# Kernel tuning notes

Measured on AMD Instinct MI355X. Metric: run time of the kernel, lower is better.

Reference implementation:

```python
import jax, jax.numpy as jnp
import numpy as np

H_HEADS = 8  # num_heads

def _layernorm(x, w, b, eps=1e-5):
    mu = x.mean(-1, keepdims=True)
    var = ((x - mu) ** 2).mean(-1, keepdims=True)
    return (x - mu) / jnp.sqrt(var + eps) * w + b

def _encoder(h, qkv_w, qkv_b, out_w, out_b, ln1_w, ln1_b, ln2_w, ln2_b, ff1_w, ff1_b, ff2_w, ff2_b):
    # h: [G, n, E]; post-norm TransformerEncoderLayer (PyTorch default, eval mode)
    G, n, E = h.shape
    hd = E // H_HEADS
    for l in range(qkv_w.shape[0]):
        qkv = h @ qkv_w[l].T + qkv_b[l]                       # [G, n, 3E]
        q, k, v = jnp.split(qkv, 3, axis=-1)
        q = q.reshape(G, n, H_HEADS, hd).transpose(0, 2, 1, 3)
        k = k.reshape(G, n, H_HEADS, hd).transpose(0, 2, 1, 3)
        v = v.reshape(G, n, H_HEADS, hd).transpose(0, 2, 1, 3)
        att = jax.nn.softmax(jnp.einsum('ghqd,ghkd->ghqk', q, k) / jnp.sqrt(jnp.float32(hd)), axis=-1)
        o = jnp.einsum('ghqk,ghkd->ghqd', att, v).transpose(0, 2, 1, 3).reshape(G, n, E)
        o = o @ out_w[l].T + out_b[l]
        h = _layernorm(h + o, ln1_w[l], ln1_b[l])
        ff = jax.nn.relu(h @ ff1_w[l].T + ff1_b[l]) @ ff2_w[l].T + ff2_b[l]
        h = _layernorm(h + ff, ln2_w[l], ln2_b[l])
    return h

def setup_inputs():
    G, N, D_IN, E, L, DFF, NE, K = 64, 512, 128, 256, 4, 2048, 524288, 128
    key = jax.random.key(0)
    ks = jax.random.split(key, 12)
    s = 0.02
    return {
        'x': jax.random.normal(ks[0], (G * N, D_IN), jnp.float32),
        'edge_index': jax.random.randint(ks[1], (2, NE), 0, G * N, dtype=jnp.int32),
        'edge_weights': jax.random.uniform(ks[2], (NE,), jnp.float32),
        'emb_w': jax.random.normal(ks[3], (E, D_IN), jnp.float32) * s,
        'emb_b': jnp.zeros((E,), jnp.float32),
        'qkv_w': jax.random.normal(ks[4], (L, 3 * E, E), jnp.float32) * s,
        'qkv_b': jnp.zeros((L, 3 * E), jnp.float32),
        'out_w': jax.random.normal(ks[5], (L, E, E), jnp.float32) * s,
        'out_b': jnp.zeros((L, E), jnp.float32),
        'ln1_w': jnp.ones((L, E), jnp.float32),
        'ln1_b': jnp.zeros((L, E), jnp.float32),
        'ln2_w': jnp.ones((L, E), jnp.float32),
        'ln2_b': jnp.zeros((L, E), jnp.float32),
        'ff1_w': jax.random.normal(ks[6], (L, DFF, E), jnp.float32) * s,
        'ff1_b': jnp.zeros((L, DFF), jnp.float32),
        'ff2_w': jax.random.normal(ks[7], (L, E, DFF), jnp.float32) * s,
        'ff2_b': jnp.zeros((L, E), jnp.float32),
        'score_w': jax.random.normal(ks[8], (1, E), jnp.float32) * s,
        'score_b': jnp.zeros((1,), jnp.float32),
        'num_graphs': 64,
        'k': 128,
    }

def reference(x, edge_index, edge_weights, emb_w, emb_b, qkv_w, qkv_b, out_w, out_b,
              ln1_w, ln1_b, ln2_w, ln2_b, ff1_w, ff1_b, ff2_w, ff2_b, score_w, score_b,
              num_graphs, k):
    GN = x.shape[0]
    n = GN // num_graphs           # uniform graph size -> node_mask == arange(G).repeat(n)
    E = emb_w.shape[0]
    h = (x @ emb_w.T + emb_b).reshape(num_graphs, n, E)
    h = _encoder(h, qkv_w, qkv_b, out_w, out_b, ln1_w, ln1_b, ln2_w, ln2_b,
                 ff1_w, ff1_b, ff2_w, ff2_b)
    scores = (h.reshape(GN, E) @ score_w.T + score_b)[:, 0]      # [GN]
    probs = jax.nn.sigmoid(scores)
    # per-graph top-k (topk_fix: k = min(sample_abs, n))
    vals, idx = jax.lax.top_k(probs.reshape(num_graphs, n), k)   # [G, k]
    full_idx = (idx + jnp.arange(num_graphs)[:, None] * n).reshape(-1)
    probs_new = jnp.zeros_like(probs).at[full_idx].set(vals.reshape(-1))
    mask = (probs_new != 0).astype(probs.dtype)
    # straight-through: indexes = detach(mask - probs) + probs; probs = probs * indexes
    indexes = jax.lax.stop_gradient(mask - probs) + probs
    probs_f = probs * indexes
    ew = edge_weights * probs_f[edge_index[0]] * probs_f[edge_index[1]]
    sampled_nodes = jnp.sort(full_idx)
    return ew, sampled_nodes, probs_f
```

## Files before the change

### kernel.cpp

```cpp
#include <hip/hip_runtime.h>
#include <cstdint>
#include <cstddef>

#define GN    32768
#define GG    64
#define NNODE 512
#define EE    256
#define LL    4
#define DFFN  2048
#define NHH   8
#define HD    32
#define NEDGE 524288
#define KSEL  128
#define DIN   128

typedef __attribute__((ext_vector_type(8))) short short8;
typedef __attribute__((ext_vector_type(4))) float floatx4;

__device__ __forceinline__ unsigned short f2bf(float x) {
  unsigned u = __float_as_uint(x);
  u = (u + 0x7FFFu + ((u >> 16) & 1u)) >> 16;
  return (unsigned short)u;
}
__device__ __forceinline__ float bf2f(unsigned short u) {
  return __uint_as_float((unsigned)u << 16);
}
__device__ __forceinline__ unsigned tpack(float v) {
  unsigned hib = __float_as_uint(v) & 0xFFFF0000u;
  float hif = __uint_as_float(hib);
  unsigned pk;
  asm("v_cvt_pk_bf16_f32 %0, %1, %2" : "=v"(pk) : "v"(hif), "v"(v - hif));
  return pk;
}
__device__ __forceinline__ unsigned short bf1(float v) {
  unsigned pk;
  asm("v_cvt_pk_bf16_f32 %0, %1, %2" : "=v"(pk) : "v"(v), "v"(0.0f));
  return (unsigned short)pk;
}
__device__ __forceinline__ void unpk(uint4 a0, uint4 a1, short8& hi, short8& lo) {
  union { short8 s; unsigned u[4]; } H, L;
  H.u[0] = __builtin_amdgcn_perm(a0.y, a0.x, 0x05040100u);
  H.u[1] = __builtin_amdgcn_perm(a0.w, a0.z, 0x05040100u);
  H.u[2] = __builtin_amdgcn_perm(a1.y, a1.x, 0x05040100u);
  H.u[3] = __builtin_amdgcn_perm(a1.w, a1.z, 0x05040100u);
  L.u[0] = __builtin_amdgcn_perm(a0.y, a0.x, 0x07060302u);
  L.u[1] = __builtin_amdgcn_perm(a0.w, a0.z, 0x07060302u);
  L.u[2] = __builtin_amdgcn_perm(a1.y, a1.x, 0x07060302u);
  L.u[3] = __builtin_amdgcn_perm(a1.w, a1.z, 0x07060302u);
  hi = H.s; lo = L.s;
}

__device__ __forceinline__ void ld_lds16(const ushort* g, ushort* l) {
  __builtin_amdgcn_global_load_lds(
      (const __attribute__((address_space(1))) unsigned int*)g,
      (__attribute__((address_space(3))) unsigned int*)l, 16, 0, 0);
}

__global__ __launch_bounds__(256) void split_kernel(const float* __restrict__ in,
                                                    ushort* __restrict__ hi,
                                                    ushort* __restrict__ lo, int n4) {
  int i = blockIdx.x * 256 + threadIdx.x;
  if (i >= n4) return;
  float4 v = ((const float4*)in)[i];
  ushort4 hv, lv;
  float t[4] = {v.x, v.y, v.z, v.w};
  unsigned short hb;
  hb = f2bf(t[0]); hv.x = hb; lv.x = f2bf(t[0] - bf2f(hb));
  hb = f2bf(t[1]); hv.y = hb; lv.y = f2bf(t[1] - bf2f(hb));
  hb = f2bf(t[2]); hv.z = hb; lv.z = f2bf(t[2] - bf2f(hb));
  hb = f2bf(t[3]); hv.w = hb; lv.w = f2bf(t[3] - bf2f(hb));
  ((ushort4*)hi)[i] = hv;
  ((ushort4*)lo)[i] = lv;
}

__global__ __launch_bounds__(256) void split_qkvw(const float* __restrict__ in,
                                                  ushort* __restrict__ hi,
                                                  ushort* __restrict__ lo, int n4) {
  int i = blockIdx.x * 256 + threadIdx.x;
  if (i >= n4) return;
  float4 v = ((const float4*)in)[i];
  int row = (i >> 6) % 768;
  float sc = (row < 256) ? (0.17677669529663687f * 1.44269504088896340f) : 1.0f;
  float t[4] = {v.x * sc, v.y * sc, v.z * sc, v.w * sc};
  ushort4 hv, lv;
  unsigned short hb;
  hb = f2bf(t[0]); hv.x = hb; lv.x = f2bf(t[0] - bf2f(hb));
  hb = f2bf(t[1]); hv.y = hb; lv.y = f2bf(t[1] - bf2f(hb));
  hb = f2bf(t[2]); hv.z = hb; lv.z = f2bf(t[2] - bf2f(hb));
  hb = f2bf(t[3]); hv.w = hb; lv.w = f2bf(t[3] - bf2f(hb));
  ((ushort4*)hi)[i] = hv;
  ((ushort4*)lo)[i] = lv;
}

__global__ __launch_bounds__(256) void scale_qb(const float* __restrict__ qb,
                                                float* __restrict__ outb) {
  int i = blockIdx.x * 256 + threadIdx.x;
  if (i >= LL * 768) return;
  float sc = ((i % 768) < 256) ? (0.17677669529663687f * 1.44269504088896340f) : 1.0f;
  outb[i] = qb[i] * sc;
}

template <int BM, int BN, int MODE, bool RELU, bool VT, bool ACC,
          bool PACKA = false, bool PACKC = false, bool SINGA = false,
          bool SINGC = false>
__global__ __launch_bounds__(256) void mm_split(
    const ushort* __restrict__ a_hi, const ushort* __restrict__ a_lo,
    const ushort* __restrict__ b_hi, const ushort* __restrict__ b_lo,
    const float* __restrict__ bias,
    float* __restrict__ Cf, ushort* __restrict__ c_hi, ushort* __restrict__ c_lo,
    ushort* __restrict__ vth, ushort* __restrict__ vtl,
    int M, int N, int K, int lda, int ldb) {
  constexpr int MI = BM / 32;
  constexpr int NJ = BN / 32;
  constexpr int APL = SINGA ? 1 : 2;
  __shared__ ushort As[2][APL][BM * 32];
  __shared__ ushort Bs[2][2][BN * 32];
  const int tid = threadIdx.x;
  const int w = tid >> 6, lane = tid & 63;
  const int wm = (w >> 1) * (BM / 2), wn = (w & 1) * (BN / 2);

  const int nwg = gridDim.x * gridDim.y;
  int flat = blockIdx.x + gridDim.x * blockIdx.y;
  int bnb, bmb;
  if ((nwg & 7) == 0) {
    int v = (flat & 7) * (nwg >> 3) + (flat >> 3);
    bnb = v % gridDim.x;
    bmb = v / gridDim.x;
  } else {
    bnb = blockIdx.x;
    bmb = blockIdx.y;
  }
  const int bm = bmb * BM, bn = bnb * BN;
  const int lrow = lane & 15, lquad = lane >> 4;

  floatx4 acc[MI][NJ];
  floatx4 zz = {0.f, 0.f, 0.f, 0.f};
#pragma unroll
  for (int i = 0; i < MI; ++i)
#pragma unroll
    for (int j = 0; j < NJ; ++j) acc[i][j] = zz;

  const uint* aP = (const uint*)a_hi;
  const int arow = tid >> 2;
  const int acol = (((tid & 3) ^ ((arow >> 1) & 3)) << 3);
  const ushort* pah = a_hi + (size_t)(bm + arow) * lda + acol;
  const ushort* pal = a_lo + (size_t)(bm + arow) * lda + acol;
  const ushort* pbh = b_hi + (size_t)(bn + arow) * ldb + acol;
  const ushort* pbl = b_lo + (size_t)(bn + arow) * ldb + acol;

  auto stage = [&](int p, int k0) {
    if constexpr (PACKA) {
#pragma unroll
      for (int s = 0; s < BM / 32; ++s) {
        int row = s * 32 + (tid >> 3);
        int gp = tid & 7;
        const uint* src = aP + (size_t)(bm + row) * lda + k0 + ((gp ^ (row & 7)) << 2);
        ld_lds16((const ushort*)src,
                 (ushort*)((char*)&As[p][0][0] + s * 4096 + tid * 16));
      }
    } else {
#pragma unroll
      for (int s = 0; s < BM / 64; ++s) {
        ld_lds16(pah + (size_t)s * 64 * lda + k0, &As[p][0][s * 2048 + tid * 8]);
        if constexpr (!SINGA)
          ld_lds16(pal + (size_t)s * 64 * lda + k0, &As[p][1][s * 2048 + tid * 8]);
      }
    }
#pragma unroll
    for (int s = 0; s < BN / 64; ++s) {
      ld_lds16(pbh + (size_t)s * 64 * ldb + k0, &Bs[p][0][s * 2048 + tid * 8]);
      ld_lds16(pbl + (size_t)s * 64 * ldb + k0, &Bs[p][1][s * 2048 + tid * 8]);
    }
  };

  stage(0, 0);
  const int nk = K >> 5;
  for (int t = 0; t < nk; ++t) {
    const int p = t & 1;
    __syncthreads();
    if (t + 1 < nk) stage(p ^ 1, (t + 1) << 5);
    short8 ah[MI], al[MI], bh[NJ], bl[NJ];
    if constexpr (PACKA) {
      const uint* Ap = (const uint*)&As[p][0][0];
#pragma unroll
      for (int i = 0; i < MI; ++i) {
        int rr = wm + i * 16 + lrow;
        const uint* rb = Ap + rr * 32;
        uint4 a0 = *(const uint4*)(rb + (((lquad * 2) ^ (rr & 7)) << 2));
        uint4 a1 = *(const uint4*)(rb + (((lquad * 2 + 1) ^ (rr & 7)) << 2));
        unpk(a0, a1, ah[i], al[i]);
      }
    } else {
#pragma unroll
      for (int i = 0; i < MI; ++i) {
        int rr = wm + i * 16 + lrow;
        int r = rr * 32 + ((lquad ^ ((rr >> 1) & 3)) << 3);
        ah[i] = *(const short8*)&As[p][0][r];
        if constexpr (!SINGA) al[i] = *(const short8*)&As[p][1][r];
      }
    }
#pragma unroll
    for (int j = 0; j < NJ; ++j) {
      int rr = wn + j * 16 + lrow;
      int r = rr * 32 + ((lquad ^ ((rr >> 1) & 3)) << 3);
      bh[j] = *(const short8*)&Bs[p][0][r];
      bl[j] = *(const short8*)&Bs[p][1][r];
    }
#pragma unroll
    for (int i = 0; i < MI; ++i)
#pragma unroll
      for (int j = 0; j < NJ; ++j) {
        if constexpr (SINGA) {
          acc[i][j] = __builtin_amdgcn_mfma_f32_16x16x32_bf16(ah[i], bl[j], acc[i][j], 0, 0, 0);
          acc[i][j] = __builtin_amdgcn_mfma_f32_16x16x32_bf16(ah[i], bh[j], acc[i][j], 0, 0, 0);
        } else {
          acc[i][j] = __builtin_amdgcn_mfma_f32_16x16x32_bf16(al[i], bh[j], acc[i][j], 0, 0, 0);
          acc[i][j] = __builtin_amdgcn_mfma_f32_16x16x32_bf16(ah[i], bl[j], acc[i][j], 0, 0, 0);
          acc[i][j] = __builtin_amdgcn_mfma_f32_16x16x32_bf16(ah[i], bh[j], acc[i][j], 0, 0, 0);
        }
      }
  }

#pragma unroll
  for (int j = 0; j < NJ; ++j) {
    int col = bn + wn + j * 16 + lrow;
    float bj = ACC ? 0.0f : bias[col];
#pragma unroll
    for (int i = 0; i < MI; ++i) {
      int row0 = bm + wm + i * 16 + lquad * 4;
#pragma unroll
      for (int r = 0; r < 4; ++r) {
        size_t off = (size_t)(row0 + r) * N + col;
        float v = acc[i][j][r] + bj;
        if constexpr (ACC) v += Cf[off];
        if (RELU) v = fmaxf(v, 0.0f);
        if constexpr (MODE & 1) Cf[off] = v;
        if constexpr (SINGC) {
          c_hi[off] = bf1(v);
        } else if constexpr (PACKC) {
          if constexpr (VT) {
            if (col < 512) {
              ((uint*)c_hi)[off] = tpack(v);
            } else {
              int hd = col - 512;
              int row = row0 + r;
              size_t vo = ((size_t)((row >> 9) * 8 + (hd >> 5)) * 32 + (hd & 31)) * 512 + (row & 511);
              vth[vo] = bf1(v);
            }
          } else {
            ((uint*)c_hi)[off] = tpack(v);
          }
        } else if constexpr (MODE & 2) {
          unsigned short hb = f2bf(v);
          unsigned short lb = f2bf(v - bf2f(hb));
          c_hi[off] = hb;
          c_lo[off] = lb;
        }
      }
    }
  }
}

__global__ __launch_bounds__(256) void mm_ln(
    const uint* __restrict__ oP,
    const ushort* __restrict__ b_hi, const ushort* __restrict__ b_lo,
    const float* __restrict__ bias, const float* __restrict__ lnw,
    const float* __restrict__ lnb, float* __restrict__ hbuf,
    uint* __restrict__ hP, int K) {
  __shared__ uint AsP[32 * 32];
  __shared__ ushort Bs[2][256 * 32];
  __shared__ float rsum[32], rsq[32], muA[32], rsA[32];
  const int tid = threadIdx.x;
  const int w = tid >> 6, lane = tid & 63;
  const int wn = w * 64;
  const int bm = blockIdx.x * 32;
  const int lr = lane & 15, quad = lane >> 4;

  floatx4 acc[2][4];
  floatx4 zz = {0.f, 0.f, 0.f, 0.f};
#pragma unroll
  for (int i = 0; i < 2; ++i)
#pragma unroll
    for (int j = 0; j < 4; ++j) acc[i][j] = zz;

  if (tid < 32) { rsum[tid] = 0.f; rsq[tid] = 0.f; }

  const int brow = tid >> 2;
  const int bcol = (((tid & 3) ^ ((brow >> 1) & 3)) << 3);

  for (int k0 = 0; k0 < K; k0 += 32) {
    __syncthreads();
    {
      int row = tid >> 3, gp = tid & 7;
      const uint* src = oP + (size_t)(bm + row) * 256 + k0 + ((gp ^ (row & 7)) << 2);
      ld_lds16((const ushort*)src, (ushort*)((char*)AsP + tid * 16));
    }
#pragma unroll
    for (int s = 0; s < 4; ++s) {
      ld_lds16(b_hi + (size_t)(s * 64 + brow) * K + bcol + k0, &Bs[0][s * 2048 + tid * 8]);
      ld_lds16(b_lo + (size_t)(s * 64 + brow) * K + bcol + k0, &Bs[1][s * 2048 + tid * 8]);
    }
    __syncthreads();
    short8 ah[2], al[2], bh[4], bl[4];
#pragma unroll
    for (int i = 0; i < 2; ++i) {
      int rr = i * 16 + lr;
      const uint* rb = AsP + rr * 32;
      uint4 a0 = *(const uint4*)(rb + (((quad * 2) ^ (rr & 7)) << 2));
      uint4 a1 = *(const uint4*)(rb + (((quad * 2 + 1) ^ (rr & 7)) << 2));
      unpk(a0, a1, ah[i], al[i]);
    }
#pragma unroll
    for (int j = 0; j < 4; ++j) {
      int rr = wn + j * 16 + lr;
      int r = rr * 32 + ((quad ^ ((rr >> 1) & 3)) << 3);
      bh[j] = *(const short8*)&Bs[0][r];
      bl[j] = *(const short8*)&Bs[1][r];
    }
#pragma unroll
    for (int i = 0; i < 2; ++i)
#pragma unroll
      for (int j = 0; j < 4; ++j) {
        acc[i][j] = __builtin_amdgcn_mfma_f32_16x16x32_bf16(al[i], bh[j], acc[i][j], 0, 0, 0);
        acc[i][j] = __builtin_amdgcn_mfma_f32_16x16x32_bf16(ah[i], bl[j], acc[i][j], 0, 0, 0);
        acc[i][j] = __builtin_amdgcn_mfma_f32_16x16x32_bf16(ah[i], bh[j], acc[i][j], 0, 0, 0);
      }
  }

#pragma unroll
  for (int i = 0; i < 2; ++i) {
#pragma unroll
    for (int r = 0; r < 4; ++r) {
      int ridx = i * 16 + quad * 4 + r;
      float sp = 0.f, qp = 0.f;
#pragma unroll
      for (int j = 0; j < 4; ++j) {
        int col = wn + j * 16 + lr;
        float v = acc[i][j][r] + bias[col] + hbuf[(size_t)(bm + ridx) * EE + col];
        acc[i][j][r] = v;
        sp += v;
        qp += v * v;
      }
#pragma unroll
      for (int m = 1; m < 16; m <<= 1) { sp += __shfl_xor(sp, m); qp += __shfl_xor(qp, m); }
      if (lr == 0) { atomicAdd(&rsum[ridx], sp); atomicAdd(&rsq[ridx], qp); }
    }
  }
  __syncthreads();
  if (tid < 32) {
    float mu = rsum[tid] * (1.0f / 256.0f);
    float var = rsq[tid] * (1.0f / 256.0f) - mu * mu;
    muA[tid] = mu;
    rsA[tid] = 1.0f / sqrtf(var + 1e-5f);
  }
  __syncthreads();
#pragma unroll
  for (int i = 0; i < 2; ++i) {
#pragma unroll
    for (int r = 0; r < 4; ++r) {
      int ridx = i * 16 + quad * 4 + r;
      float mu = muA[ridx], rsv = rsA[ridx];
#pragma unroll
      for (int j = 0; j < 4; ++j) {
        int col = wn + j * 16 + lr;
        float o = (acc[i][j][r] - mu) * rsv * lnw[col] + lnb[col];
        size_t off = (size_t)(bm + ridx) * EE + col;
        hbuf[off] = o;
        hP[off] = tpack(o);
      }
    }
  }
}

__global__ __launch_bounds__(256) void ln_res_kernel(float* __restrict__ h,
                                                     const float* __restrict__ t,
                                                     const float* __restrict__ w,
                                                     const float* __restrict__ b,
                                                     uint* __restrict__ hP) {
  int row = blockIdx.x * 4 + (threadIdx.x >> 6);
  int lane = threadIdx.x & 63;
  size_t off = (size_t)row * EE + (lane << 2);
  float4 hv = *(const float4*)&h[off];
  float4 tv = *(const float4*)&t[off];
  float v0 = hv.x + tv.x, v1 = hv.y + tv.y, v2 = hv.z + tv.z, v3 = hv.w + tv.w;
  float s = (v0 + v1) + (v2 + v3);
#pragma unroll
  for (int m = 32; m > 0; m >>= 1) s += __shfl_xor(s, m);
  float mu = s * (1.0f / 256.0f);
  float d0 = v0 - mu, d1 = v1 - mu, d2 = v2 - mu, d3 = v3 - mu;
  float s2 = (d0 * d0 + d1 * d1) + (d2 * d2 + d3 * d3);
#pragma unroll
  for (int m = 32; m > 0; m >>= 1) s2 += __shfl_xor(s2, m);
  float rs = 1.0f / sqrtf(s2 * (1.0f / 256.0f) + 1e-5f);
  float4 wv = *(const float4*)&w[lane << 2];
  float4 bv = *(const float4*)&b[lane << 2];
  float4 o;
  o.x = d0 * rs * wv.x + bv.x;
  o.y = d1 * rs * wv.y + bv.y;
  o.z = d2 * rs * wv.z + bv.z;
  o.w = d3 * rs * wv.w + bv.w;
  *(float4*)&h[off] = o;
  uint4 pk;
  pk.x = tpack(o.x);
  pk.y = tpack(o.y);
  pk.z = tpack(o.z);
  pk.w = tpack(o.w);
  *(uint4*)&hP[off] = pk;
}

__global__ __launch_bounds__(256) void attn_mfma(const uint* __restrict__ qP,
                                                 const ushort* __restrict__ vtS,
                                                 uint* __restrict__ oP) {
  __shared__ ushort Ks[2][64 * 40];
  __shared__ ushort Vt[32 * 72];
  __shared__ ushort Ps[4][16 * 72];
  const int tid = threadIdx.x;
  const int w = tid >> 6, lane = tid & 63, c = lane & 15, quad = lane >> 4;
  int flat = blockIdx.x + 8 * (blockIdx.y + 8 * blockIdx.z);
  int v = (flat & 7) * ((GG * 64) >> 3) + (flat >> 3);
  const int qt = v & 7, hh = (v >> 3) & 7, g = v >> 6;
  const size_t g512 = (size_t)g * 512;
  const size_t vtbase = (size_t)(g * 8 + hh) * 32 * 512;

  const size_t qnode = g512 + qt * 64 + w * 16 + c;
  const uint* qp0 = qP + qnode * 768 + hh * 32 + quad * 8;
  uint4 q0 = *(const uint4*)qp0, q1 = *(const uint4*)(qp0 + 4);
  short8 qfh, qfl;
  unpk(q0, q1, qfh, qfl);

  floatx4 O0 = {0.f, 0.f, 0.f, 0.f}, O1 = {0.f, 0.f, 0.f, 0.f};
  floatx4 Lac = {0.f, 0.f, 0.f, 0.f};
  const short onev = (short)0x3F80;
  const short8 onef = {onev, onev, onev, onev, onev, onev, onev, onev};

  const int skey = tid >> 2, sdc = (tid & 3) << 3;
  const int sd = tid >> 3, skc = (tid & 7) << 3;
  uint4 stg[2];
  short8 stgv;
  auto load_tile = [&](int kb) {
    size_t go = (g512 + kb + skey) * 768 + 256 + hh * 32 + sdc;
    stg[0] = *(const uint4*)(qP + go);
    stg[1] = *(const uint4*)(qP + go + 4);
    size_t vo = vtbase + (size_t)sd * 512 + kb + skc;
    stgv = *(const short8*)(vtS + vo);
  };
  load_tile(0);

  for (int t = 0; t < 8; ++t) {
    if (t) __syncthreads();
    {
      short8 kh, kl;
      unpk(stg[0], stg[1], kh, kl);
      *(short8*)&Ks[0][skey * 40 + sdc] = kh;
      *(short8*)&Ks[1][skey * 40 + sdc] = kl;
      *(short8*)&Vt[sd * 72 + skc] = stgv;
    }
    __syncthreads();
    if (t < 7) load_tile((t + 1) * 64);

    floatx4 S[4];
#pragma unroll
    for (int n = 0; n < 4; ++n) {
      int r = (n * 16 + c) * 40 + quad * 8;
      short8 kfh = *(const short8*)&Ks[0][r];
      short8 kfl = *(const short8*)&Ks[1][r];
      floatx4 s = {0.f, 0.f, 0.f, 0.f};
      s = __builtin_amdgcn_mfma_f32_16x16x32_bf16(qfh, kfl, s, 0, 0, 0);
      s = __builtin_amdgcn_mfma_f32_16x16x32_bf16(qfl, kfh, s, 0, 0, 0);
      s = __builtin_amdgcn_mfma_f32_16x16x32_bf16(qfh, kfh, s, 0, 0, 0);
      S[n] = s;
    }
#pragma unroll
    for (int n = 0; n < 4; ++n) {
#pragma unroll
      for (int r = 0; r < 4; ++r) {
        float pp = exp2f(S[n][r]);
        Ps[w][(quad * 4 + r) * 72 + n * 16 + c] = bf1(pp);
      }
    }
#pragma unroll
    for (int ks = 0; ks < 2; ++ks) {
      short8 p = *(const short8*)&Ps[w][c * 72 + ks * 32 + quad * 8];
      short8 v0 = *(const short8*)&Vt[c * 72 + ks * 32 + quad * 8];
      short8 v1 = *(const short8*)&Vt[(16 + c) * 72 + ks * 32 + quad * 8];
      O0 = __builtin_amdgcn_mfma_f32_16x16x32_bf16(p, v0, O0, 0, 0, 0);
      O1 = __builtin_amdgcn_mfma_f32_16x16x32_bf16(p, v1, O1, 0, 0, 0);
      Lac = __builtin_amdgcn_mfma_f32_16x16x32_bf16(p, onef, Lac, 0, 0, 0);
    }
  }

#pragma unroll
  for (int r = 0; r < 4; ++r) {
    float inv = 1.0f / Lac[r];
    size_t node = g512 + qt * 64 + w * 16 + quad * 4 + r;
    size_t off0 = node * EE + hh * 32 + c;
    oP[off0] = tpack(O0[r] * inv);
    oP[off0 + 16] = tpack(O1[r] * inv);
  }
}

__global__ __launch_bounds__(256) void score_kernel(const float* __restrict__ h,
                                                    const float* __restrict__ sw,
                                                    const float* __restrict__ sb,
                                                    float* __restrict__ probs) {
  int row = blockIdx.x * 4 + (threadIdx.x >> 6);
  int lane = threadIdx.x & 63;
  float4 a = *(const float4*)&h[(size_t)row * EE + (lane << 2)];
  float4 w = *(const float4*)&sw[lane << 2];
  float s = (a.x * w.x + a.y * w.y) + (a.z * w.z + a.w * w.w);
#pragma unroll
  for (int m = 32; m > 0; m >>= 1) s += __shfl_xor(s, m);
  if (lane == 0) {
    float sc = s + sb[0];
    probs[row] = 1.0f / (1.0f + expf(-sc));
  }
}

__global__ __launch_bounds__(256) void topk_kernel(const float* __restrict__ probs,
                                                   float* __restrict__ out) {
  __shared__ unsigned long long keys[NNODE];
  __shared__ float pv[NNODE];
  __shared__ int flags[NNODE];
  __shared__ int sc[NNODE];
  const int g = blockIdx.x, tid = threadIdx.x;
  for (int i = tid; i < NNODE; i += 256) {
    float p = probs[g * NNODE + i];
    pv[i] = p;
    keys[i] = ((unsigned long long)__float_as_uint(p) << 32) |
              (unsigned long long)(~(unsigned)i);
    flags[i] = 0;
  }
  for (int k = 2; k <= NNODE; k <<= 1) {
    for (int j = k >> 1; j > 0; j >>= 1) {
      __syncthreads();
      for (int i = tid; i < NNODE; i += 256) {
        int ixj = i ^ j;
        if (ixj > i) {
          unsigned long long a = keys[i], bq = keys[ixj];
          bool desc = ((i & k) == 0);
          bool sw = desc ? (a < bq) : (a > bq);
          if (sw) { keys[i] = bq; keys[ixj] = a; }
        }
      }
    }
  }
  __syncthreads();
  if (tid < KSEL) {
    unsigned idx = ~(unsigned)(keys[tid] & 0xFFFFFFFFull);
    flags[idx] = 1;
  }
  __syncthreads();
  sc[tid] = flags[tid];
  sc[tid + 256] = flags[tid + 256];
  for (int off = 1; off < NNODE; off <<= 1) {
    __syncthreads();
    int x0 = (tid >= off) ? sc[tid - off] : 0;
    int x1 = sc[tid + 256 - off];
    int b0 = sc[tid], b1 = sc[tid + 256];
    __syncthreads();
    sc[tid] = b0 + x0;
    sc[tid + 256] = b1 + x1;
  }
  __syncthreads();
  for (int i = tid; i < NNODE; i += 256) {
    float p = pv[i];
    int f = flags[i];
    float ind = ((float)f - p) + p;
    float pf = p * ind;
    out[NEDGE + GG * KSEL + g * NNODE + i] = pf;
    if (f) out[NEDGE + g * KSEL + (sc[i] - 1)] = (float)(g * NNODE + i);
  }
}

__global__ __launch_bounds__(256) void edge_kernel(const int* __restrict__ ei,
                                                   const float* __restrict__ w,
                                                   float* __restrict__ out) {
  int e = blockIdx.x * 256 + threadIdx.x;
  const float* pf = out + NEDGE + GG * KSEL;
  out[e] = w[e] * pf[ei[e]] * pf[ei[NEDGE + e]];
}

extern "C" void kernel_launch(void* const* d_in, const int* in_sizes, int n_in,
                              void* d_out, int out_size, void* d_ws, size_t ws_size,
                              hipStream_t stream) {
  (void)in_sizes; (void)n_in; (void)out_size; (void)ws_size;
  const float* x     = (const float*)d_in[0];
  const int*   ei    = (const int*)d_in[1];
  const float* ewts  = (const float*)d_in[2];
  const float* emb_w = (const float*)d_in[3];
  const float* emb_b = (const float*)d_in[4];
  const float* qkv_w = (const float*)d_in[5];
  const float* qkv_b = (const float*)d_in[6];
  const float* out_w = (const float*)d_in[7];
  const float* out_b = (const float*)d_in[8];
  const float* ln1_w = (const float*)d_in[9];
  const float* ln1_b = (const float*)d_in[10];
  const float* ln2_w = (const float*)d_in[11];
  const float* ln2_b = (const float*)d_in[12];
  const float* ff1_w = (const float*)d_in[13];
  const float* ff1_b = (const float*)d_in[14];
  const float* ff2_w = (const float*)d_in[15];
  const float* ff2_b = (const float*)d_in[16];
  const float* sc_w  = (const float*)d_in[17];
  const float* sc_b  = (const float*)d_in[18];
  float* out = (float*)d_out;

  const size_t MB = 1024 * 1024;
  char* base = (char*)d_ws;
  float*  h    = (float*)base;
  uint*   hP   = (uint*)(base + 32 * MB);
  char*   R    = base + 64 * MB;
  uint*   qkvP = (uint*)R;
  uint*   oP   = (uint*)(R + 96 * MB);
  ushort* vtS  = (ushort*)(R + 128 * MB);
  ushort* tS   = (ushort*)R;
  float*  delta = (float*)(R + 128 * MB);
  ushort* x_hi = (ushort*)R;
  ushort* x_lo = (ushort*)(R + 8 * MB);
  float*  probs = (float*)R;
  char* W = base + 224 * MB;
  size_t woff = 0;
  auto walloc = [&](size_t bytes) { char* r = W + woff; woff += (bytes + 255) & ~(size_t)255; return (ushort*)r; };
  ushort* we_hi = walloc(256 * 128 * 2);
  ushort* we_lo = walloc(256 * 128 * 2);
  ushort* wq_hi = walloc((size_t)LL * 768 * 256 * 2);
  ushort* wq_lo = walloc((size_t)LL * 768 * 256 * 2);
  ushort* wo_hi = walloc((size_t)LL * 256 * 256 * 2);
  ushort* wo_lo = walloc((size_t)LL * 256 * 256 * 2);
  ushort* w1_hi = walloc((size_t)LL * DFFN * 256 * 2);
  ushort* w1_lo = walloc((size_t)LL * DFFN * 256 * 2);
  ushort* w2_hi = walloc((size_t)LL * 256 * DFFN * 2);
  ushort* w2_lo = walloc((size_t)LL * 256 * DFFN * 2);
  float*  qbs   = (float*)walloc((size_t)LL * 768 * 4);

  auto split = [&](const float* src, ushort* hi, ushort* lo, size_t n) {
    int n4 = (int)(n / 4);
    split_kernel<<<(n4 + 255) / 256, 256, 0, stream>>>(src, hi, lo, n4);
  };
  split(x, x_hi, x_lo, (size_t)GN * DIN);
  split(emb_w, we_hi, we_lo, 256 * 128);
  split_qkvw<<<((LL * 768 * 256 / 4) + 255) / 256, 256, 0, stream>>>(
      qkv_w, wq_hi, wq_lo, LL * 768 * 256 / 4);
  scale_qb<<<(LL * 768 + 255) / 256, 256, 0, stream>>>(qkv_b, qbs);
  split(out_w, wo_hi, wo_lo, (size_t)LL * 256 * 256);
  split(ff1_w, w1_hi, w1_lo, (size_t)LL * DFFN * 256);
  split(ff2_w, w2_hi, w2_lo, (size_t)LL * 256 * DFFN);

  mm_split<128, 128, 1, false, false, false, false, true><<<dim3(EE / 128, GN / 128), 256, 0, stream>>>(
      x_hi, x_lo, we_hi, we_lo, emb_b, h, (ushort*)hP, nullptr, nullptr, nullptr,
      GN, EE, DIN, DIN, DIN);

  for (int l = 0; l < LL; ++l) {
    mm_split<128, 128, 0, false, true, false, true, true><<<dim3(768 / 128, GN / 128), 256, 0, stream>>>(
        (const ushort*)hP, nullptr, wq_hi + (size_t)l * 768 * 256, wq_lo + (size_t)l * 768 * 256,
        qbs + l * 768, nullptr, (ushort*)qkvP, nullptr, vtS, nullptr,
        GN, 768, EE, EE, EE);
    attn_mfma<<<dim3(8, 8, GG), 256, 0, stream>>>(qkvP, vtS, oP);
    mm_ln<<<GN / 32, 256, 0, stream>>>(
        oP, wo_hi + (size_t)l * 256 * 256, wo_lo + (size_t)l * 256 * 256,
        out_b + l * 256, ln1_w + l * EE, ln1_b + l * EE, h, hP, EE);
    for (int s = 0; s < 2; ++s) {
      mm_split<128, 128, 0, true, false, false, true, false, false, true><<<dim3(1024 / 128, GN / 128), 256, 0, stream>>>(
          (const ushort*)hP, nullptr,
          w1_hi + (size_t)l * DFFN * 256 + (size_t)s * 1024 * 256,
          w1_lo + (size_t)l * DFFN * 256 + (size_t)s * 1024 * 256,
          ff1_b + l * DFFN + s * 1024, nullptr, tS, nullptr, nullptr, nullptr,
          GN, 1024, EE, EE, EE);
      if (s == 0)
        mm_split<128, 128, 1, false, false, false, false, false, true><<<dim3(EE / 128, GN / 128), 256, 0, stream>>>(
            tS, nullptr,
            w2_hi + (size_t)l * 256 * DFFN, w2_lo + (size_t)l * 256 * DFFN,
            ff2_b + l * 256, delta, nullptr, nullptr, nullptr, nullptr,
            GN, EE, 1024, 1024, DFFN);
      else
        mm_split<128, 128, 1, false, false, true, false, false, true><<<dim3(EE / 128, GN / 128), 256, 0, stream>>>(
            tS, nullptr,
            w2_hi + (size_t)l * 256 * DFFN + 1024, w2_lo + (size_t)l * 256 * DFFN + 1024,
            ff2_b + l * 256, delta, nullptr, nullptr, nullptr, nullptr,
            GN, EE, 1024, 1024, DFFN);
    }
    ln_res_kernel<<<GN / 4, 256, 0, stream>>>(
        h, delta, ln2_w + l * EE, ln2_b + l * EE, hP);
  }

  score_kernel<<<GN / 4, 256, 0, stream>>>(h, sc_w, sc_b, probs);
  topk_kernel<<<GG, 256, 0, stream>>>(probs, out);
  edge_kernel<<<NEDGE / 256, 256, 0, stream>>>(ei, ewts, out);
}
```

Baseline: 1.730 ms.

## Run FFN matmuls in single-pass fp16 MFMA instead of split bf16

The two feed-forward GEMMs per layer switch from the split-bf16 scheme (2 MFMAs per tile with a single-plane A) to a new fp16 GEMM kernel that issues one fp16 MFMA per tile. FF weights are converted once to fp16, the LN1 kernel additionally writes an fp16 copy of h, and the FF1 intermediate is stored as fp16. This halves the MFMA work and the weight-plane loads in the dominant FFN GEMMs, at the cost of lower precision on weights (fp16 mantissa instead of hi/lo bf16) and an extra fp16 write in mm_ln. Buffer placement is reshuffled to fit the new h16 buffer.

```diff
diff --git a/kernel.cpp b/kernel.cpp
--- a/kernel.cpp
+++ b/kernel.cpp
@@ -16,6 +16,8 @@
 
 typedef __attribute__((ext_vector_type(8))) short short8;
 typedef __attribute__((ext_vector_type(4))) float floatx4;
+typedef _Float16 half8 __attribute__((ext_vector_type(8)));
+union h8u { short8 s; half8 h; };
 
 __device__ __forceinline__ unsigned short f2bf(float x) {
   unsigned u = __float_as_uint(x);
@@ -36,6 +38,11 @@
   unsigned pk;
   asm("v_cvt_pk_bf16_f32 %0, %1, %2" : "=v"(pk) : "v"(v), "v"(0.0f));
   return (unsigned short)pk;
+}
+__device__ __forceinline__ unsigned short f2h(float x) {
+  union { _Float16 f; unsigned short u; } c;
+  c.f = (_Float16)x;
+  return c.u;
 }
 __device__ __forceinline__ void unpk(uint4 a0, uint4 a1, short8& hi, short8& lo) {
   union { short8 s; unsigned u[4]; } H, L;
@@ -71,6 +78,16 @@
   hb = f2bf(t[3]); hv.w = hb; lv.w = f2bf(t[3] - bf2f(hb));
   ((ushort4*)hi)[i] = hv;
   ((ushort4*)lo)[i] = lv;
+}
+
+__global__ __launch_bounds__(256) void split_f16(const float* __restrict__ in,
+                                                 ushort* __restrict__ o, int n4) {
+  int i = blockIdx.x * 256 + threadIdx.x;
+  if (i >= n4) return;
+  float4 v = ((const float4*)in)[i];
+  ushort4 r;
+  r.x = f2h(v.x); r.y = f2h(v.y); r.z = f2h(v.z); r.w = f2h(v.w);
+  ((ushort4*)o)[i] = r;
 }
 
 __global__ __launch_bounds__(256) void split_qkvw(const float* __restrict__ in,
@@ -101,8 +118,7 @@
 }
 
 template <int BM, int BN, int MODE, bool RELU, bool VT, bool ACC,
-          bool PACKA = false, bool PACKC = false, bool SINGA = false,
-          bool SINGC = false>
+          bool PACKA = false, bool PACKC = false>
 __global__ __launch_bounds__(256) void mm_split(
     const ushort* __restrict__ a_hi, const ushort* __restrict__ a_lo,
     const ushort* __restrict__ b_hi, const ushort* __restrict__ b_lo,
@@ -112,8 +128,7 @@
     int M, int N, int K, int lda, int ldb) {
   constexpr int MI = BM / 32;
   constexpr int NJ = BN / 32;
-  constexpr int APL = SINGA ? 1 : 2;
-  __shared__ ushort As[2][APL][BM * 32];
+  __shared__ ushort As[2][2][BM * 32];
   __shared__ ushort Bs[2][2][BN * 32];
   const int tid = threadIdx.x;
   const int w = tid >> 6, lane = tid & 63;
@@ -162,8 +177,7 @@
 #pragma unroll
       for (int s = 0; s < BM / 64; ++s) {
         ld_lds16(pah + (size_t)s * 64 * lda + k0, &As[p][0][s * 2048 + tid * 8]);
-        if constexpr (!SINGA)
-          ld_lds16(pal + (size_t)s * 64 * lda + k0, &As[p][1][s * 2048 + tid * 8]);
+        ld_lds16(pal + (size_t)s * 64 * lda + k0, &As[p][1][s * 2048 + tid * 8]);
       }
     }
 #pragma unroll
@@ -196,7 +210,7 @@
         int rr = wm + i * 16 + lrow;
         int r = rr * 32 + ((lquad ^ ((rr >> 1) & 3)) << 3);
         ah[i] = *(const short8*)&As[p][0][r];
-        if constexpr (!SINGA) al[i] = *(const short8*)&As[p][1][r];
+        al[i] = *(const short8*)&As[p][1][r];
       }
     }
 #pragma unroll
@@ -210,14 +224,9 @@
     for (int i = 0; i < MI; ++i)
 #pragma unroll
       for (int j = 0; j < NJ; ++j) {
-        if constexpr (SINGA) {
-          acc[i][j] = __builtin_amdgcn_mfma_f32_16x16x32_bf16(ah[i], bl[j], acc[i][j], 0, 0, 0);
-          acc[i][j] = __builtin_amdgcn_mfma_f32_16x16x32_bf16(ah[i], bh[j], acc[i][j], 0, 0, 0);
-        } else {
-          acc[i][j] = __builtin_amdgcn_mfma_f32_16x16x32_bf16(al[i], bh[j], acc[i][j], 0, 0, 0);
-          acc[i][j] = __builtin_amdgcn_mfma_f32_16x16x32_bf16(ah[i], bl[j], acc[i][j], 0, 0, 0);
-          acc[i][j] = __builtin_amdgcn_mfma_f32_16x16x32_bf16(ah[i], bh[j], acc[i][j], 0, 0, 0);
-        }
+        acc[i][j] = __builtin_amdgcn_mfma_f32_16x16x32_bf16(al[i], bh[j], acc[i][j], 0, 0, 0);
+        acc[i][j] = __builtin_amdgcn_mfma_f32_16x16x32_bf16(ah[i], bl[j], acc[i][j], 0, 0, 0);
+        acc[i][j] = __builtin_amdgcn_mfma_f32_16x16x32_bf16(ah[i], bh[j], acc[i][j], 0, 0, 0);
       }
   }
 
@@ -235,9 +244,7 @@
         if constexpr (ACC) v += Cf[off];
         if (RELU) v = fmaxf(v, 0.0f);
         if constexpr (MODE & 1) Cf[off] = v;
-        if constexpr (SINGC) {
-          c_hi[off] = bf1(v);
-        } else if constexpr (PACKC) {
+        if constexpr (PACKC) {
           if constexpr (VT) {
             if (col < 512) {
               ((uint*)c_hi)[off] = tpack(v);
@@ -261,12 +268,101 @@
   }
 }
 
+template <bool RELU, bool ACC, bool OUT16>
+__global__ __launch_bounds__(256) void mm_f16(
+    const ushort* __restrict__ a16, const ushort* __restrict__ b16,
+    const float* __restrict__ bias,
+    float* __restrict__ Cf, ushort* __restrict__ c16,
+    int M, int N, int K, int lda, int ldb) {
+  __shared__ ushort As[2][128 * 32];
+  __shared__ ushort Bs[2][128 * 32];
+  const int tid = threadIdx.x;
+  const int w = tid >> 6, lane = tid & 63;
+  const int wm = (w >> 1) * 64, wn = (w & 1) * 64;
+
+  const int nwg = gridDim.x * gridDim.y;
+  int flat = blockIdx.x + gridDim.x * blockIdx.y;
+  int bnb, bmb;
+  if ((nwg & 7) == 0) {
+    int v = (flat & 7) * (nwg >> 3) + (flat >> 3);
+    bnb = v % gridDim.x;
+    bmb = v / gridDim.x;
+  } else {
+    bnb = blockIdx.x;
+    bmb = blockIdx.y;
+  }
+  const int bm = bmb * 128, bn = bnb * 128;
+  const int lrow = lane & 15, lquad = lane >> 4;
+
+  floatx4 acc[4][4];
+  floatx4 zz = {0.f, 0.f, 0.f, 0.f};
+#pragma unroll
+  for (int i = 0; i < 4; ++i)
+#pragma unroll
+    for (int j = 0; j < 4; ++j) acc[i][j] = zz;
+
+  const int arow = tid >> 2;
+  const int acol = (((tid & 3) ^ ((arow >> 1) & 3)) << 3);
+  const ushort* pa = a16 + (size_t)(bm + arow) * lda + acol;
+  const ushort* pb = b16 + (size_t)(bn + arow) * ldb + acol;
+
+  auto stage = [&](int p, int k0) {
+    ld_lds16(pa + k0, &As[p][tid * 8]);
+    ld_lds16(pa + (size_t)64 * lda + k0, &As[p][2048 + tid * 8]);
+    ld_lds16(pb + k0, &Bs[p][tid * 8]);
+    ld_lds16(pb + (size_t)64 * ldb + k0, &Bs[p][2048 + tid * 8]);
+  };
+
+  stage(0, 0);
+  const int nk = K >> 5;
+  for (int t = 0; t < nk; ++t) {
+    const int p = t & 1;
+    __syncthreads();
+    if (t + 1 < nk) stage(p ^ 1, (t + 1) << 5);
+    h8u a[4], b[4];
+#pragma unroll
+    for (int i = 0; i < 4; ++i) {
+      int rr = wm + i * 16 + lrow;
+      a[i].s = *(const short8*)&As[p][rr * 32 + ((lquad ^ ((rr >> 1) & 3)) << 3)];
+    }
+#pragma unroll
+    for (int j = 0; j < 4; ++j) {
+      int rr = wn + j * 16 + lrow;
+      b[j].s = *(const short8*)&Bs[p][rr * 32 + ((lquad ^ ((rr >> 1) & 3)) << 3)];
+    }
+#pragma unroll
+    for (int i = 0; i < 4; ++i)
+#pragma unroll
+      for (int j = 0; j < 4; ++j)
+        acc[i][j] = __builtin_amdgcn_mfma_f32_16x16x32_f16(a[i].h, b[j].h, acc[i][j], 0, 0, 0);
+  }
+
+#pragma unroll
+  for (int j = 0; j < 4; ++j) {
+    int col = bn + wn + j * 16 + lrow;
+    float bj = ACC ? 0.0f : bias[col];
+#pragma unroll
+    for (int i = 0; i < 4; ++i) {
+      int row0 = bm + wm + i * 16 + lquad * 4;
+#pragma unroll
+      for (int r = 0; r < 4; ++r) {
+        size_t off = (size_t)(row0 + r) * N + col;
+        float v = acc[i][j][r] + bj;
+        if constexpr (ACC) v += Cf[off];
+        if (RELU) v = fmaxf(v, 0.0f);
+        if constexpr (OUT16) c16[off] = f2h(v);
+        else Cf[off] = v;
+      }
+    }
+  }
+}
+
 __global__ __launch_bounds__(256) void mm_ln(
     const uint* __restrict__ oP,
     const ushort* __restrict__ b_hi, const ushort* __restrict__ b_lo,
     const float* __restrict__ bias, const float* __restrict__ lnw,
     const float* __restrict__ lnb, float* __restrict__ hbuf,
-    uint* __restrict__ hP, int K) {
+    uint* __restrict__ hP, ushort* __restrict__ h16, int K) {
   __shared__ uint AsP[32 * 32];
   __shared__ ushort Bs[2][256 * 32];
   __shared__ float rsum[32], rsq[32], muA[32], rsA[32];
@@ -367,6 +463,7 @@
         size_t off = (size_t)(bm + ridx) * EE + col;
         hbuf[off] = o;
         hP[off] = tpack(o);
+        h16[off] = f2h(o);
       }
     }
   }
@@ -613,8 +710,9 @@
   uint*   qkvP = (uint*)R;
   uint*   oP   = (uint*)(R + 96 * MB);
   ushort* vtS  = (ushort*)(R + 128 * MB);
-  ushort* tS   = (ushort*)R;
-  float*  delta = (float*)(R + 128 * MB);
+  ushort* h16  = (ushort*)(R + 144 * MB);
+  ushort* t16  = (ushort*)R;
+  float*  delta = (float*)(R + 96 * MB);
   ushort* x_hi = (ushort*)R;
   ushort* x_lo = (ushort*)(R + 8 * MB);
   float*  probs = (float*)R;
@@ -627,11 +725,9 @@
   ushort* wq_lo = walloc((size_t)LL * 768 * 256 * 2);
   ushort* wo_hi = walloc((size_t)LL * 256 * 256 * 2);
   ushort* wo_lo = walloc((size_t)LL * 256 * 256 * 2);
-  ushort* w1_hi = walloc((size_t)LL * DFFN * 256 * 2);
-  ushort* w1_lo = walloc((size_t)LL * DFFN * 256 * 2);
-  ushort* w2_hi = walloc((size_t)LL * 256 * DFFN * 2);
-  ushort* w2_lo = walloc((size_t)LL * 256 * DFFN * 2);
-  float*  qbs   = (float*)walloc((size_t)LL * 768 * 4);
+  ushort* w1f = walloc((size_t)LL * DFFN * 256 * 2);
+  ushort* w2f = walloc((size_t)LL * 256 * DFFN * 2);
+  float*  qbs = (float*)walloc((size_t)LL * 768 * 4);
 
   auto split = [&](const float* src, ushort* hi, ushort* lo, size_t n) {
     int n4 = (int)(n / 4);
@@ -643,8 +739,10 @@
       qkv_w, wq_hi, wq_lo, LL * 768 * 256 / 4);
   scale_qb<<<(LL * 768 + 255) / 256, 256, 0, stream>>>(qkv_b, qbs);
   split(out_w, wo_hi, wo_lo, (size_t)LL * 256 * 256);
-  split(ff1_w, w1_hi, w1_lo, (size_t)LL * DFFN * 256);
-  split(ff2_w, w2_hi, w2_lo, (size_t)LL * 256 * DFFN);
+  split_f16<<<((LL * DFFN * 256 / 4) + 255) / 256, 256, 0, stream>>>(
+      ff1_w, w1f, LL * DFFN * 256 / 4);
+  split_f16<<<((LL * 256 * DFFN / 4) + 255) / 256, 256, 0, stream>>>(
+      ff2_w, w2f, LL * 256 * DFFN / 4);
 
   mm_split<128, 128, 1, false, false, false, false, true><<<dim3(EE / 128, GN / 128), 256, 0, stream>>>(
       x_hi, x_lo, we_hi, we_lo, emb_b, h, (ushort*)hP, nullptr, nullptr, nullptr,
@@ -658,25 +756,21 @@
     attn_mfma<<<dim3(8, 8, GG), 256, 0, stream>>>(qkvP, vtS, oP);
     mm_ln<<<GN / 32, 256, 0, stream>>>(
         oP, wo_hi + (size_t)l * 256 * 256, wo_lo + (size_t)l * 256 * 256,
-        out_b + l * 256, ln1_w + l * EE, ln1_b + l * EE, h, hP, EE);
+        out_b + l * 256, ln1_w + l * EE, ln1_b + l * EE, h, hP, h16, EE);
     for (int s = 0; s < 2; ++s) {
-      mm_split<128, 128, 0, true, false, false, true, false, false, true><<<dim3(1024 / 128, GN / 128), 256, 0, stream>>>(
-          (const ushort*)hP, nullptr,
-          w1_hi + (size_t)l * DFFN * 256 + (size_t)s * 1024 * 256,
-          w1_lo + (size_t)l * DFFN * 256 + (size_t)s * 1024 * 256,
-          ff1_b + l * DFFN + s * 1024, nullptr, tS, nullptr, nullptr, nullptr,
+      mm_f16<true, false, true><<<dim3(1024 / 128, GN / 128), 256, 0, stream>>>(
+          h16, w1f + (size_t)l * DFFN * 256 + (size_t)s * 1024 * 256,
+          ff1_b + l * DFFN + s * 1024, nullptr, t16,
           GN, 1024, EE, EE, EE);
       if (s == 0)
-        mm_split<128, 128, 1, false, false, false, false, false, true><<<dim3(EE / 128, GN / 128), 256, 0, stream>>>(
-            tS, nullptr,
-            w2_hi + (size_t)l * 256 * DFFN, w2_lo + (size_t)l * 256 * DFFN,
-            ff2_b + l * 256, delta, nullptr, nullptr, nullptr, nullptr,
+        mm_f16<false, false, false><<<dim3(EE / 128, GN / 128), 256, 0, stream>>>(
+            t16, w2f + (size_t)l * 256 * DFFN,
+            ff2_b + l * 256, delta, nullptr,
             GN, EE, 1024, 1024, DFFN);
       else
-        mm_split<128, 128, 1, false, false, true, false, false, true><<<dim3(EE / 128, GN / 128), 256, 0, stream>>>(
-            tS, nullptr,
-            w2_hi + (size_t)l * 256 * DFFN + 1024, w2_lo + (size_t)l * 256 * DFFN + 1024,
-            ff2_b + l * 256, delta, nullptr, nullptr, nullptr, nullptr,
+        mm_f16<false, true, false><<<dim3(EE / 128, GN / 128), 256, 0, stream>>>(
+            t16, w2f + (size_t)l * 256 * DFFN + 1024,
+            ff2_b + l * 256, delta, nullptr,
             GN, EE, 1024, 1024, DFFN);
     }
     ln_res_kernel<<<GN / 4, 256, 0, stream>>>(
```

After: 1.484 ms. 14.2% less time.
